# Kernel optimization log

Hardware: AMD Instinct MI355X
Metric: run time of the kernel (lower is better)

The kernel has to match this reference:

```python
import jax, jax.numpy as jnp
import numpy as np

BATCH, IN_SIZE, CH, DIM, MODES, LAYERS, PROJ, OUT = 16, 1, 128, 128, 32, 4, 128, 1


def setup_inputs() -> dict:
    key = jax.random.key(0)
    ks = jax.random.split(key, 12)
    scale = 1.0 / (CH * CH)
    inp = {
        "z": jax.random.normal(ks[0], (BATCH, IN_SIZE, DIM, DIM), dtype=jnp.float32),
        # Lifting: pointwise linear input_size -> channels
        "lift_w": jax.random.normal(ks[1], (CH, IN_SIZE), dtype=jnp.float32) / np.sqrt(IN_SIZE),
        "lift_b": jnp.zeros((CH,), dtype=jnp.float32),
        # Spectral conv weights per layer, two mode corners, complex stored as real/imag
        "wr1": scale * jax.random.normal(ks[2], (LAYERS, CH, CH, MODES, MODES), dtype=jnp.float32),
        "wi1": scale * jax.random.normal(ks[3], (LAYERS, CH, CH, MODES, MODES), dtype=jnp.float32),
        "wr2": scale * jax.random.normal(ks[4], (LAYERS, CH, CH, MODES, MODES), dtype=jnp.float32),
        "wi2": scale * jax.random.normal(ks[5], (LAYERS, CH, CH, MODES, MODES), dtype=jnp.float32),
        # Projection: channels -> projection_size -> output_size (pointwise MLP)
        "pw1": jax.random.normal(ks[6], (PROJ, CH), dtype=jnp.float32) / np.sqrt(CH),
        "pb1": jnp.zeros((PROJ,), dtype=jnp.float32),
        "pw2": jax.random.normal(ks[7], (OUT, PROJ), dtype=jnp.float32) / np.sqrt(PROJ),
        "pb2": jnp.zeros((OUT,), dtype=jnp.float32),
    }
    return inp


def _spectral_conv(v, w1, w2, modes, size):
    # v: [b, c, X, Y] real; rfft2 over last two dims (norm='backward')
    vf = jnp.fft.rfft2(v, norm="backward")  # [b, c, X, Y//2+1] complex
    of = jnp.zeros_like(vf)
    # low-frequency corner
    of = of.at[:, :, :modes, :modes].set(
        jnp.einsum("bixy,ioxy->boxy", vf[:, :, :modes, :modes], w1))
    # high (negative) frequency corner along first spatial axis
    of = of.at[:, :, -modes:, :modes].set(
        jnp.einsum("bixy,ioxy->boxy", vf[:, :, -modes:, :modes], w2))
    return jnp.fft.irfft2(of, s=(size, size), norm="backward")


def reference(z, lift_w, lift_b, wr1, wi1, wr2, wi2, pw1, pb1, pw2, pb2):
    n_layers = wr1.shape[0]
    modes = wr1.shape[-1]
    size = z.shape[-1]
    # Lifting: [b, in, x, y] -> [b, ch, x, y]
    v = jnp.einsum("bixy,ci->bcxy", z, lift_w) + lift_b[None, :, None, None]
    out = v
    for l in range(n_layers):
        w1 = wr1[l] + 1j * wi1[l]
        w2 = wr2[l] + 1j * wi2[l]
        out = _spectral_conv(out, w1, w2, modes, size)
    # Projection MLP (pointwise over grid)
    h = jnp.einsum("bcxy,pc->bpxy", out, pw1) + pb1[None, :, None, None]
    h = jax.nn.gelu(h)
    out = jnp.einsum("bpxy,op->boxy", h, pw2) + pb2[None, :, None, None]
    return out
```

## Files before the change

### kernel.cpp

```cpp
#include <hip/hip_runtime.h>
#include <math.h>

#define B 16
#define CH 128
#define DIM 128
#define MODES 32
#define NLAYERS 4
#define PROJ 128
#define U 64
#define KY 32
#define NMODE (U*KY)
#define N2 (DIM*DIM)
#define PG 32
#define PPG (PROJ/PG)

__device__ __forceinline__ void async16(const void* g, void* l) {
  __builtin_amdgcn_global_load_lds((const __attribute__((address_space(1))) unsigned int*)g,
                                   (__attribute__((address_space(3))) unsigned int*)l, 16, 0, 0);
}

__global__ __launch_bounds__(256) void k_zf1(const float* __restrict__ z,
                                             float2* __restrict__ t1) {
  __shared__ float zrow[16][DIM];
  __shared__ float2 tw[DIM];
  int bid = blockIdx.x;
  int b = bid >> 3, xt = bid & 7;
  int x0 = xt * 16;
  int t = threadIdx.x;
  if (t < 128) {
    float ang = (float)(2.0 * M_PI) * (float)t / 128.0f;
    tw[t] = make_float2(cosf(ang), sinf(ang));
  }
  for (int e = t; e < 16 * DIM / 4; e += 256)
    ((float4*)&zrow[0][0])[e] = ((const float4*)&z[b * N2 + x0 * DIM])[e];
  __syncthreads();
  #pragma unroll
  for (int j = 0; j < 2; ++j) {
    int it = t + j * 256;
    int x_l = it >> 5, ky = it & 31;
    float tr = 0.f, ti = 0.f;
    for (int y = 0; y < DIM; ++y) {
      float v = zrow[x_l][y];
      float2 w = tw[(ky * y) & 127];
      tr += v * w.x;
      ti -= v * w.y;
    }
    t1[((size_t)b * DIM + x0 + x_l) * KY + ky] = make_float2(tr, ti);
  }
}

__global__ __launch_bounds__(256) void k_zf2(const float2* __restrict__ t1,
                                             float* __restrict__ zfr, float* __restrict__ zfi) {
  __shared__ float2 t1s[DIM][KY];
  __shared__ float2 tw[DIM];
  int bid = blockIdx.x;
  int b = bid >> 1, uh = bid & 1;
  int t = threadIdx.x;
  if (t < 128) {
    float ang = (float)(2.0 * M_PI) * (float)t / 128.0f;
    tw[t] = make_float2(cosf(ang), sinf(ang));
  }
  for (int e = t; e < DIM * KY / 2; e += 256)
    ((float4*)&t1s[0][0])[e] = ((const float4*)&t1[(size_t)b * DIM * KY])[e];
  __syncthreads();
  #pragma unroll
  for (int j = 0; j < 4; ++j) {
    int m = t + j * 256;
    int u_l = m >> 5, ky = m & 31;
    int u = uh * 32 + u_l;
    int kx = (u < 32) ? u : (u + 64);
    float ar = 0.f, ai = 0.f;
    for (int x = 0; x < DIM; ++x) {
      float2 v = t1s[x][ky];
      float2 w = tw[(kx * x) & 127];
      ar += v.x * w.x + v.y * w.y;
      ai += v.y * w.x - v.x * w.y;
    }
    zfr[b * NMODE + u * KY + ky] = ar;
    zfi[b * NMODE + u * KY + ky] = ai;
  }
}

__global__ __launch_bounds__(256) void k_lift(const float* __restrict__ zfr, const float* __restrict__ zfi,
                                              const float* __restrict__ lw, const float* __restrict__ lb,
                                              float2* __restrict__ vcout) {
  int idx = blockIdx.x * 256 + threadIdx.x;
  if (idx >= B * CH * NMODE) return;
  int m = idx & (NMODE - 1);
  int c = (idx >> 11) & 127;
  int b = idx >> 18;
  float w = lw[c];
  float re = w * zfr[b * NMODE + m];
  float im = w * zfi[b * NMODE + m];
  if (m == 0) re += 16384.f * lb[c];
  vcout[idx] = make_float2(re, im);
}

__global__ __launch_bounds__(256) void k_spec(const float2* __restrict__ vc,
                                              const float* __restrict__ wr1, const float* __restrict__ wi1,
                                              const float* __restrict__ wr2, const float* __restrict__ wi2,
                                              float2* __restrict__ oc) {
  __shared__ float  lW[2][2][2][16][16];
  __shared__ float2 lV[2][2][16][16];
  int bid = blockIdx.x;
  int u = ((bid & 7) << 3) | ((bid >> 3) & 7);
  int rest = bid >> 6;
  int ot = rest & 7, kyh = rest >> 3;
  int o0 = ot * 16;
  int ky0 = kyh * 16;
  int kxw = u & 31;
  const float* wr = (u >= 32) ? wr2 : wr1;
  const float* wi = (u >= 32) ? wi2 : wi1;
  int t = threadIdx.x;
  int ky = t & 15, oh = (t >> 4) & 3, bq = t >> 6;
  int wv = t >> 6, lane = t & 63;
  float accR[4][4] = {}, accI[4][4] = {};

  #define STAGE(bf, i0)                                                              \
    {                                                                                \
      _Pragma("unroll")                                                              \
      for (int n = 0; n < 2; ++n) {                                                  \
        int nu = wv * 2 + n;                                                         \
        if (nu < 4) {                                                                \
          int ri = nu >> 1, il = nu & 1;                                             \
          int o_l = lane >> 2, kyq = lane & 3;                                       \
          const float* src = (ri ? wi : wr) +                                        \
            (((size_t)((i0) + il) * CH + o0 + o_l) * MODES + kxw) * MODES +          \
            ky0 + kyq * 4;                                                           \
          async16(src, (char*)&lW[bf][0][0][0][0] + (size_t)nu * 1024 + lane * 16);  \
        } else {                                                                     \
          int nv = nu - 4;                                                           \
          int il = nv >> 1, bhf = nv & 1;                                            \
          int b_l = bhf * 8 + (lane >> 3), kyd = lane & 7;                           \
          const float2* src = vc + ((size_t)b_l * CH + (i0) + il) * NMODE +          \
                              u * KY + ky0 + kyd * 2;                                \
          async16(src, (char*)&lV[bf][0][0][0] + (size_t)nv * 1024 + lane * 16);     \
        }                                                                            \
      }                                                                              \
    }

  #define COMPUTE(bf)                                                                \
    {                                                                                \
      _Pragma("unroll")                                                              \
      for (int il = 0; il < 2; ++il) {                                               \
        float wrv[4], wiv[4];                                                        \
        _Pragma("unroll")                                                            \
        for (int j = 0; j < 4; ++j) {                                                \
          wrv[j] = lW[bf][0][il][oh * 4 + j][ky];                                    \
          wiv[j] = lW[bf][1][il][oh * 4 + j][ky];                                    \
        }                                                                            \
        _Pragma("unroll")                                                            \
        for (int bb = 0; bb < 4; ++bb) {                                             \
          float2 v = lV[bf][il][bq * 4 + bb][ky];                                    \
          _Pragma("unroll")                                                          \
          for (int j = 0; j < 4; ++j) {                                              \
            accR[j][bb] += wrv[j] * v.x - wiv[j] * v.y;                              \
            accI[j][bb] += wrv[j] * v.y + wiv[j] * v.x;                              \
          }                                                                          \
        }                                                                            \
      }                                                                              \
    }

  STAGE(0, 0);
  for (int k = 0; k < 64; ++k) {
    int cur = k & 1;
    __syncthreads();
    if (k + 1 < 64) STAGE(cur ^ 1, (k + 1) * 2);
    COMPUTE(cur);
  }
  #undef STAGE
  #undef COMPUTE
  #pragma unroll
  for (int j = 0; j < 4; ++j)
    #pragma unroll
    for (int bb = 0; bb < 4; ++bb) {
      int o = o0 + oh * 4 + j, b = bq * 4 + bb;
      oc[(((size_t)b * CH + o) * U + u) * KY + ky0 + ky] = make_float2(accR[j][bb], accI[j][bb]);
    }
}

__global__ __launch_bounds__(256) void k_proj0(float2* __restrict__ vc) {
  int idx = blockIdx.x * 256 + threadIdx.x;
  if (idx >= B * CH * 33) return;
  int pi = idx % 33;
  int bc = idx / 33;
  float2* base = vc + (size_t)bc * NMODE;
  if (pi == 0) {
    base[0].y = 0.f;
  } else if (pi == 32) {
    base[32 * KY].x *= 0.5f;
    base[32 * KY].y *= 0.5f;
  } else {
    int ua = pi, ub = 64 - pi;
    float2 a = base[ua * KY], b2 = base[ub * KY];
    base[ua * KY] = make_float2(0.5f * (a.x + b2.x), 0.5f * (a.y - b2.y));
    base[ub * KY] = make_float2(0.5f * (b2.x + a.x), 0.5f * (b2.y - a.y));
  }
}

__global__ __launch_bounds__(256) void k_pw1(const float2* __restrict__ xc,
                                             const float* __restrict__ pw1,
                                             float2* __restrict__ hc) {
  __shared__ float wT[CH][CH + 1];
  int bid = blockIdx.x;
  int b = ((bid & 7) << 1) | ((bid >> 8) & 1);
  int jt = (bid >> 3) & 31;
  int t = threadIdx.x;
  for (int e = t; e < CH * CH; e += 256) {
    int p = e >> 7, c = e & 127;
    wT[c][p] = pw1[e];
  }
  __syncthreads();
  int tx = t & 15, ty = t >> 4;
  int j0 = jt * 64 + tx * 4;
  float accR[4][8] = {}, accI[4][8] = {};
  for (int c = 0; c < CH; ++c) {
    const float4* x4 = (const float4*)&xc[((size_t)b * CH + c) * NMODE + j0];
    float4 v0 = x4[0], v1 = x4[1];
    float xrv[4] = {v0.x, v0.z, v1.x, v1.z};
    float xiv[4] = {v0.y, v0.w, v1.y, v1.w};
    float w[8];
    #pragma unroll
    for (int pp = 0; pp < 8; ++pp) w[pp] = wT[c][ty * 8 + pp];
    #pragma unroll
    for (int jj = 0; jj < 4; ++jj)
      #pragma unroll
      for (int pp = 0; pp < 8; ++pp) {
        accR[jj][pp] += w[pp] * xrv[jj];
        accI[jj][pp] += w[pp] * xiv[jj];
      }
  }
  #pragma unroll
  for (int pp = 0; pp < 8; ++pp) {
    int p = ty * 8 + pp;
    float4* o4 = (float4*)&hc[((size_t)b * CH + p) * NMODE + j0];
    o4[0] = make_float4(accR[0][pp], accI[0][pp], accR[1][pp], accI[1][pp]);
    o4[1] = make_float4(accR[2][pp], accI[2][pp], accR[3][pp], accI[3][pp]);
  }
}

__global__ __launch_bounds__(256) void k_idft_partial(const float2* __restrict__ hc,
                                                      const float* __restrict__ pb1,
                                                      const float* __restrict__ pw2,
                                                      float* __restrict__ partial) {
  __shared__ float2 tw[DIM];
  __shared__ float2 hfs[2][NMODE];
  __shared__ float2 sbuf[16][KY];
  __shared__ float4 sE[8][32];
  int bid = blockIdx.x;
  int b = (bid & 7) | (((bid >> 3) & 1) << 3);
  int pg = (bid >> 4) & 31, xs = bid >> 9;
  int x0 = xs * 8;
  int t = threadIdx.x;
  int wv = t >> 6, lane = t & 63;
  if (t < 128) {
    float ang = (float)(2.0 * M_PI) * (float)t / 128.0f;
    tw[t] = make_float2(cosf(ang), sinf(ang));
  }

  #define STAGE_H(bf, pp_)                                                           \
    {                                                                                \
      const char* srcb = (const char*)(hc + ((size_t)b * CH + pg * PPG + (pp_)) * NMODE); \
      _Pragma("unroll")                                                              \
      for (int n = 0; n < 4; ++n) {                                                  \
        int nu = wv * 4 + n;                                                         \
        async16(srcb + (size_t)nu * 1024 + lane * 16,                                \
                (char*)&hfs[bf][0] + (size_t)nu * 1024 + lane * 16);                 \
      }                                                                              \
    }

  STAGE_H(0, 0);
  __syncthreads();
  {
    int xq = t >> 5, j = t & 31;
    int x = x0 + xq;
    int kxE = (j < 16) ? (2 * j) : (2 * j + 64);
    float2 wE = tw[(kxE * x) & 127];
    float2 wO = tw[((kxE + 1) * x) & 127];
    sE[xq][j] = make_float4(wE.x, wE.y, wO.x, wO.y);
  }
  int y = t & 63, xh = t >> 6;
  float Cr[KY], Sr[KY];
  #pragma unroll
  for (int ky = 0; ky < KY; ++ky) {
    float2 w = tw[(ky * y) & 127];
    float wk = (ky == 0) ? 1.f : 2.f;
    Cr[ky] = wk * w.x;
    Sr[ky] = -wk * w.y;
  }
  __syncthreads();
  int xqA = t >> 5, kyA = t & 31;
  float res[8] = {0.f, 0.f, 0.f, 0.f, 0.f, 0.f, 0.f, 0.f};
  for (int pp = 0; pp < PPG; ++pp) {
    int p = pg * PPG + pp;
    int cur = pp & 1;
    if (pp) __syncthreads();
    if (pp + 1 < PPG) STAGE_H(cur ^ 1, pp + 1);
    {
      float per = 0.f, pei = 0.f, por = 0.f, poi = 0.f;
      #pragma unroll
      for (int j = 0; j < 32; ++j) {
        float4 E = sE[xqA][j];
        float2 h0 = hfs[cur][(2 * j) * KY + kyA];
        float2 h1 = hfs[cur][(2 * j + 1) * KY + kyA];
        per += h0.x * E.x - h0.y * E.y;
        pei += h0.x * E.y + h0.y * E.x;
        por += h1.x * E.z - h1.y * E.w;
        poi += h1.x * E.w + h1.y * E.z;
      }
      sbuf[xqA][kyA]     = make_float2(per + por, pei + poi);
      sbuf[xqA + 8][kyA] = make_float2(per - por, pei - poi);
    }
    __syncthreads();
    float pb = pb1[p], pw = pw2[p];
    #pragma unroll
    for (int sl = 0; sl < 4; ++sl) {
      int s_i = xh + sl * 4;
      float ae = 0.f, ao = 0.f;
      #pragma unroll
      for (int ky = 0; ky < KY; ky += 2) {
        float4 v = *(const float4*)&sbuf[s_i][ky];
        ae += v.x * Cr[ky] + v.y * Sr[ky];
        ao += v.z * Cr[ky + 1] + v.w * Sr[ky + 1];
      }
      float hlo = (ae + ao) * (1.f / 16384.f) + pb;
      float hhi = (ae - ao) * (1.f / 16384.f) + pb;
      float zlo = 1.5957691216057308f * (hlo + 0.044715f * hlo * hlo * hlo);
      float zhi = 1.5957691216057308f * (hhi + 0.044715f * hhi * hhi * hhi);
      res[sl * 2]     += pw * hlo * __builtin_amdgcn_rcpf(1.f + __expf(-zlo));
      res[sl * 2 + 1] += pw * hhi * __builtin_amdgcn_rcpf(1.f + __expf(-zhi));
    }
  }
  #undef STAGE_H
  size_t pbase = ((size_t)pg * B + b) * N2;
  #pragma unroll
  for (int sl = 0; sl < 4; ++sl) {
    int s_i = xh + sl * 4;
    int x = x0 + (s_i & 7) + ((s_i >> 3) << 6);
    partial[pbase + x * DIM + y]      = res[sl * 2];
    partial[pbase + x * DIM + y + 64] = res[sl * 2 + 1];
  }
}

__global__ __launch_bounds__(256) void k_reduce(const float* __restrict__ partial,
                                                const float* __restrict__ pb2,
                                                float* __restrict__ outp) {
  int idx = blockIdx.x * 256 + threadIdx.x;
  if (idx >= B * N2) return;
  float s = pb2[0];
  #pragma unroll
  for (int pg = 0; pg < PG; ++pg) s += partial[(size_t)pg * B * N2 + idx];
  outp[idx] = s;
}

extern "C" void kernel_launch(void* const* d_in, const int* in_sizes, int n_in,
                              void* d_out, int out_size, void* d_ws, size_t ws_size,
                              hipStream_t stream) {
  const float* z   = (const float*)d_in[0];
  const float* lw  = (const float*)d_in[1];
  const float* lb  = (const float*)d_in[2];
  const float* wr1 = (const float*)d_in[3];
  const float* wi1 = (const float*)d_in[4];
  const float* wr2 = (const float*)d_in[5];
  const float* wi2 = (const float*)d_in[6];
  const float* pw1 = (const float*)d_in[7];
  const float* pb1 = (const float*)d_in[8];
  const float* pw2 = (const float*)d_in[9];
  const float* pb2 = (const float*)d_in[10];
  float* out = (float*)d_out;
  float* ws = (float*)d_ws;

  float* zfr = ws;
  float* zfi = zfr + 32768;
  float2* Ac = (float2*)(ws + 65536);
  float2* Bc = Ac + (size_t)B * CH * NMODE;
  float2* t1 = Bc;

  k_zf1<<<B * 8, 256, 0, stream>>>(z, t1);
  k_zf2<<<B * 2, 256, 0, stream>>>(t1, zfr, zfi);
  k_lift<<<(B * CH * NMODE) / 256, 256, 0, stream>>>(zfr, zfi, lw, lb, Ac);

  const size_t WSTRIDE = (size_t)CH * CH * MODES * MODES;
  float2 *ir = Ac, *oc = Bc;
  for (int l = 0; l < NLAYERS; ++l) {
    k_spec<<<1024, 256, 0, stream>>>(ir,
                                     wr1 + l * WSTRIDE, wi1 + l * WSTRIDE,
                                     wr2 + l * WSTRIDE, wi2 + l * WSTRIDE,
                                     oc);
    if (l < NLAYERS - 1)
      k_proj0<<<(B * CH * 33 + 255) / 256, 256, 0, stream>>>(oc);
    float2* tmp = ir; ir = oc; oc = tmp;
  }
  k_pw1<<<512, 256, 0, stream>>>(ir, pw1, oc);
  float* partial = (float*)ir;
  k_idft_partial<<<B * PG * 8, 256, 0, stream>>>(oc, pb1, pw2, partial);
  k_reduce<<<(B * N2) / 256, 256, 0, stream>>>(partial, pb2, out);
}
```

Before: 770.9 us.

## Split spectral contraction over input channels with full ky tile and combine pass

```diff
diff --git a/kernel.cpp b/kernel.cpp
--- a/kernel.cpp
+++ b/kernel.cpp
@@ -96,10 +96,102 @@
   vcout[idx] = make_float2(re, im);
 }
 
-__global__ __launch_bounds__(256) void k_spec(const float2* __restrict__ vc,
-                                              const float* __restrict__ wr1, const float* __restrict__ wi1,
-                                              const float* __restrict__ wr2, const float* __restrict__ wi2,
-                                              float2* __restrict__ oc) {
+__global__ __launch_bounds__(256) void k_spec_ih(const float2* __restrict__ vc,
+                                                 const float* __restrict__ wr1, const float* __restrict__ wi1,
+                                                 const float* __restrict__ wr2, const float* __restrict__ wi2,
+                                                 float2* __restrict__ pc0, float2* __restrict__ pc1) {
+  __shared__ float4 lds[2][1024];
+  int bid = blockIdx.x;
+  int u = ((bid & 7) << 3) | ((bid >> 3) & 7);
+  int rest = bid >> 6;
+  int ot = rest & 7, ih = rest >> 3;
+  int o0 = ot * 16;
+  int i0 = ih * 64;
+  int kxw = u & 31;
+  const float* wr = (u >= 32) ? wr2 : wr1;
+  const float* wi = (u >= 32) ? wi2 : wi1;
+  float2* pc = ih ? pc1 : pc0;
+  int t = threadIdx.x;
+  int ky = t & 31, bh = (t >> 5) & 1, wv = t >> 6;
+  int lane = t & 63;
+  float accR[4][8] = {}, accI[4][8] = {};
+
+  #define STAGE(bf, c)                                                               \
+    {                                                                                \
+      char* dstW = (char*)&lds[bf][0];                                               \
+      char* dstV = dstW + 8192;                                                      \
+      int ib = i0 + (c) * 2;                                                         \
+      _Pragma("unroll")                                                              \
+      for (int n = 0; n < 4; ++n) {                                                  \
+        int nu = wv * 4 + n;                                                         \
+        if (nu < 8) {                                                                \
+          int row = nu * 8 + (lane >> 3);                                            \
+          int ri = row >> 5, il = (row >> 4) & 1, o_l = row & 15;                    \
+          const float* src = (ri ? wi : wr) +                                        \
+            ((size_t)(ib + il) * CH + o0 + o_l) * 1024 + kxw * 32 + (lane & 7) * 4;  \
+          async16(src, dstW + (size_t)nu * 1024 + lane * 16);                        \
+        } else {                                                                     \
+          int nv = nu - 8;                                                           \
+          int row4 = nv * 4 + (lane >> 4);                                           \
+          int il = row4 >> 4, b_l = row4 & 15;                                       \
+          const float2* src = vc + ((size_t)b_l * CH + ib + il) * NMODE +            \
+                              u * KY + (lane & 15) * 2;                              \
+          async16(src, dstV + (size_t)nv * 1024 + lane * 16);                        \
+        }                                                                            \
+      }                                                                              \
+    }
+
+  STAGE(0, 0);
+  for (int k = 0; k < 32; ++k) {
+    int cur = k & 1;
+    __syncthreads();
+    if (k + 1 < 32) STAGE(cur ^ 1, k + 1);
+    {
+      const float*  Wb = (const float*)&lds[cur][0];
+      const float2* Vb = (const float2*)((const char*)&lds[cur][0] + 8192);
+      #pragma unroll
+      for (int il = 0; il < 2; ++il) {
+        float wrv[4], wiv[4];
+        #pragma unroll
+        for (int j = 0; j < 4; ++j) {
+          wrv[j] = Wb[(il * 16 + wv * 4 + j) * 32 + ky];
+          wiv[j] = Wb[(32 + il * 16 + wv * 4 + j) * 32 + ky];
+        }
+        #pragma unroll
+        for (int bb = 0; bb < 8; ++bb) {
+          float2 v = Vb[(il * 16 + bh * 8 + bb) * 32 + ky];
+          #pragma unroll
+          for (int j = 0; j < 4; ++j) {
+            accR[j][bb] += wrv[j] * v.x - wiv[j] * v.y;
+            accI[j][bb] += wrv[j] * v.y + wiv[j] * v.x;
+          }
+        }
+      }
+    }
+  }
+  #undef STAGE
+  #pragma unroll
+  for (int j = 0; j < 4; ++j)
+    #pragma unroll
+    for (int bb = 0; bb < 8; ++bb) {
+      int o = o0 + wv * 4 + j, b = bh * 8 + bb;
+      pc[(((size_t)b * CH + o) * U + u) * KY + ky] = make_float2(accR[j][bb], accI[j][bb]);
+    }
+}
+
+__global__ __launch_bounds__(256) void k_combine(const float2* __restrict__ pc1,
+                                                 float2* __restrict__ oc) {
+  int idx = blockIdx.x * 256 + threadIdx.x;
+  const float4* a = (const float4*)pc1;
+  float4* o = (float4*)oc;
+  float4 va = a[idx], vo = o[idx];
+  o[idx] = make_float4(vo.x + va.x, vo.y + va.y, vo.z + va.z, vo.w + va.w);
+}
+
+__global__ __launch_bounds__(256) void k_spec_fb(const float2* __restrict__ vc,
+                                                 const float* __restrict__ wr1, const float* __restrict__ wi1,
+                                                 const float* __restrict__ wr2, const float* __restrict__ wi2,
+                                                 float2* __restrict__ oc) {
   __shared__ float  lW[2][2][2][16][16];
   __shared__ float2 lV[2][2][16][16];
   int bid = blockIdx.x;
@@ -115,7 +207,6 @@
   int ky = t & 15, oh = (t >> 4) & 3, bq = t >> 6;
   int wv = t >> 6, lane = t & 63;
   float accR[4][4] = {}, accI[4][4] = {};
-
   #define STAGE(bf, i0)                                                              \
     {                                                                                \
       _Pragma("unroll")                                                              \
@@ -138,38 +229,33 @@
         }                                                                            \
       }                                                                              \
     }
-
-  #define COMPUTE(bf)                                                                \
-    {                                                                                \
-      _Pragma("unroll")                                                              \
-      for (int il = 0; il < 2; ++il) {                                               \
-        float wrv[4], wiv[4];                                                        \
-        _Pragma("unroll")                                                            \
-        for (int j = 0; j < 4; ++j) {                                                \
-          wrv[j] = lW[bf][0][il][oh * 4 + j][ky];                                    \
-          wiv[j] = lW[bf][1][il][oh * 4 + j][ky];                                    \
-        }                                                                            \
-        _Pragma("unroll")                                                            \
-        for (int bb = 0; bb < 4; ++bb) {                                             \
-          float2 v = lV[bf][il][bq * 4 + bb][ky];                                    \
-          _Pragma("unroll")                                                          \
-          for (int j = 0; j < 4; ++j) {                                              \
-            accR[j][bb] += wrv[j] * v.x - wiv[j] * v.y;                              \
-            accI[j][bb] += wrv[j] * v.y + wiv[j] * v.x;                              \
-          }                                                                          \
-        }                                                                            \
-      }                                                                              \
-    }
-
   STAGE(0, 0);
   for (int k = 0; k < 64; ++k) {
     int cur = k & 1;
     __syncthreads();
     if (k + 1 < 64) STAGE(cur ^ 1, (k + 1) * 2);
-    COMPUTE(cur);
+    {
+      #pragma unroll
+      for (int il = 0; il < 2; ++il) {
+        float wrv[4], wiv[4];
+        #pragma unroll
+        for (int j = 0; j < 4; ++j) {
+          wrv[j] = lW[cur][0][il][oh * 4 + j][ky];
+          wiv[j] = lW[cur][1][il][oh * 4 + j][ky];
+        }
+        #pragma unroll
+        for (int bb = 0; bb < 4; ++bb) {
+          float2 v = lV[cur][il][bq * 4 + bb][ky];
+          #pragma unroll
+          for (int j = 0; j < 4; ++j) {
+            accR[j][bb] += wrv[j] * v.x - wiv[j] * v.y;
+            accI[j][bb] += wrv[j] * v.y + wiv[j] * v.x;
+          }
+        }
+      }
+    }
   }
   #undef STAGE
-  #undef COMPUTE
   #pragma unroll
   for (int j = 0; j < 4; ++j)
     #pragma unroll
@@ -370,10 +456,14 @@
   float* out = (float*)d_out;
   float* ws = (float*)d_ws;
 
+  const size_t CBUF = (size_t)B * CH * NMODE;
   float* zfr = ws;
   float* zfi = zfr + 32768;
   float2* Ac = (float2*)(ws + 65536);
-  float2* Bc = Ac + (size_t)B * CH * NMODE;
+  float2* Bc = Ac + CBUF;
+  float2* Pc = Bc + CBUF;
+  const size_t need3 = 65536u * 4 + 3ull * CBUF * 8;
+  const bool big = ws_size >= need3;
   float2* t1 = Bc;
 
   k_zf1<<<B * 8, 256, 0, stream>>>(z, t1);
@@ -383,10 +473,18 @@
   const size_t WSTRIDE = (size_t)CH * CH * MODES * MODES;
   float2 *ir = Ac, *oc = Bc;
   for (int l = 0; l < NLAYERS; ++l) {
-    k_spec<<<1024, 256, 0, stream>>>(ir,
-                                     wr1 + l * WSTRIDE, wi1 + l * WSTRIDE,
-                                     wr2 + l * WSTRIDE, wi2 + l * WSTRIDE,
-                                     oc);
+    if (big) {
+      k_spec_ih<<<1024, 256, 0, stream>>>(ir,
+                                          wr1 + l * WSTRIDE, wi1 + l * WSTRIDE,
+                                          wr2 + l * WSTRIDE, wi2 + l * WSTRIDE,
+                                          oc, Pc);
+      k_combine<<<(int)(CBUF / 2 / 256), 256, 0, stream>>>(Pc, oc);
+    } else {
+      k_spec_fb<<<1024, 256, 0, stream>>>(ir,
+                                          wr1 + l * WSTRIDE, wi1 + l * WSTRIDE,
+                                          wr2 + l * WSTRIDE, wi2 + l * WSTRIDE,
+                                          oc);
+    }
     if (l < NLAYERS - 1)
       k_proj0<<<(B * CH * 33 + 255) / 256, 256, 0, stream>>>(oc);
     float2* tmp = ir; ir = oc; oc = tmp;
```

Measured after the change: 855.3 us. +11.0%, slower.
